# Kernel tuning notes

Measured on AMD Instinct MI355X. Metric: run time of the kernel, lower is better.

## Reference

```python
import jax, jax.numpy as jnp
import numpy as np

N, E, F, H, EA = 50000, 640000, 128, 128, 8


def setup_inputs() -> dict:
    key = jax.random.key(0)
    ks = jax.random.split(key, 16)
    s = 0.05
    return {
        "h": jax.random.normal(ks[0], (N, F), jnp.float32),
        "pos": jax.random.normal(ks[1], (N, 3), jnp.float32),
        "edge_index": jax.random.randint(ks[2], (2, E), 0, N, jnp.int32),
        "edge_attr": jax.random.normal(ks[3], (E, EA), jnp.float32),
        # edge_mlp_1: in = 2F + 1 + EA
        "eW1": jax.random.normal(ks[4], (2 * F + 1 + EA, H), jnp.float32) * s,
        "eb1": jnp.zeros((H,), jnp.float32),
        "eW2": jax.random.normal(ks[5], (H, H), jnp.float32) * s,
        "eb2": jnp.zeros((H,), jnp.float32),
        "aW": jax.random.normal(ks[6], (H, 1), jnp.float32) * s,
        "ab": jnp.zeros((1,), jnp.float32),
        "nW1": jax.random.normal(ks[7], (H + F, H), jnp.float32) * s,
        "nb1": jnp.zeros((H,), jnp.float32),
        "nW2": jax.random.normal(ks[8], (H, F), jnp.float32) * s,
        "nb2": jnp.zeros((F,), jnp.float32),
        # pos_mlp_2: xavier with gain 0.001 -> tiny init, no bias
        "pW2": jax.random.normal(ks[9], (H, 1), jnp.float32) * 0.001,
    }


def reference(h, pos, edge_index, edge_attr,
              eW1, eb1, eW2, eb2, aW, ab,
              nW1, nb1, nW2, nb2, pW2):
    n = h.shape[0]
    row, col = edge_index[0], edge_index[1]
    # radial info
    pos_diff = pos[row] - pos[col]                      # [E,3]
    dist_sq = jnp.sum(pos_diff * pos_diff, axis=-1, keepdims=True)  # [E,1]
    # edge model (Eq.3): gather -> MLP -> sigmoid attention gate
    e_in = jnp.concatenate([h[row], h[col], dist_sq, edge_attr], axis=-1)
    m = jax.nn.silu(e_in @ eW1 + eb1)
    m = jax.nn.silu(m @ eW2 + eb2)
    m = m * jax.nn.sigmoid(m @ aW + ab)                 # [E,H]
    # pos model (note: original overwrites pos_mlp_1 output; faithful to that)
    trans = pos_diff * (m @ pW2)                        # [E,3]
    agg_t = jax.ops.segment_sum(trans, row, num_segments=n)
    cnt = jax.ops.segment_sum(jnp.ones((trans.shape[0], 1), trans.dtype), row,
                              num_segments=n)
    pos_new = pos + agg_t / jnp.maximum(cnt, 1.0)       # unsorted_segment_mean
    # node model: scatter-sum aggregate -> MLP -> residual
    agg = jax.ops.segment_sum(m, row, num_segments=n)   # [N,H]
    o = jax.nn.silu(jnp.concatenate([h, agg], axis=1) @ nW1 + nb1)
    h_new = o @ nW2 + nb2 + h
    return h_new, pos_new, m
```

## Files before the change

### kernel.cpp

```cpp
#include <hip/hip_runtime.h>
#include <hip/hip_bf16.h>

#define NN 50000
#define EE 640000
#define FF 128
#define HH 128

typedef unsigned short ushort_t;
typedef unsigned int   uint_t;
using f32x4  = __attribute__((ext_vector_type(4))) float;
using bf16x8 = __attribute__((ext_vector_type(8))) __bf16;
using u16x8  = __attribute__((ext_vector_type(8))) unsigned short;

__device__ __forceinline__ ushort_t f2bf(float f) {
    union { float f; unsigned int i; } v; v.f = f;
    unsigned int r = v.i + 0x7fffu + ((v.i >> 16) & 1u);
    return (ushort_t)(r >> 16);
}
__device__ __forceinline__ float bf2f(uint_t u) {
    union { uint_t i; float f; } v; v.i = u << 16; return v.f;
}
__device__ __forceinline__ float fsilu(float x) { return x / (1.f + __expf(-x)); }
__device__ __forceinline__ float fsig(float x)  { return 1.f / (1.f + __expf(-x)); }

__device__ __forceinline__ u16x8 cvt8(const float* p) {
    float4 a0 = *reinterpret_cast<const float4*>(p);
    float4 a1 = *reinterpret_cast<const float4*>(p + 4);
    u16x8 v;
    v[0] = f2bf(a0.x); v[1] = f2bf(a0.y); v[2] = f2bf(a0.z); v[3] = f2bf(a0.w);
    v[4] = f2bf(a1.x); v[5] = f2bf(a1.y); v[6] = f2bf(a1.z); v[7] = f2bf(a1.w);
    return v;
}

__global__ void prep_kernel(const float* __restrict__ h, ushort_t* __restrict__ hbf,
                            const int* __restrict__ eidx, int* __restrict__ deg)
{
    const int t = blockIdx.x * 256 + threadIdx.x;
    if (t * 8 < NN * 128) {
        u16x8 v = cvt8(h + (size_t)t * 8);
        *reinterpret_cast<u16x8*>(hbf + (size_t)t * 8) = v;
    }
    if (t < EE) atomicAdd(&deg[eidx[t]], 1);
}

__global__ void scan_kernel(const int* __restrict__ deg, int* __restrict__ row_ptr,
                            int* __restrict__ cursor)
{
    __shared__ int sdata[1024];
    const int t = threadIdx.x;
    const int chunk = (NN + 1023) / 1024;
    const int start = t * chunk;
    const int end   = min(start + chunk, NN);
    int s = 0;
    for (int i = start; i < end; ++i) s += deg[i];
    sdata[t] = s;
    __syncthreads();
    for (int off = 1; off < 1024; off <<= 1) {
        int v = (t >= off) ? sdata[t - off] : 0;
        __syncthreads();
        sdata[t] += v;
        __syncthreads();
    }
    int ox = sdata[t] - s;
    for (int i = start; i < end; ++i) {
        row_ptr[i] = ox; cursor[i] = ox; ox += deg[i];
    }
    if (t == 1023) row_ptr[NN] = sdata[1023];
}

__global__ void scatter_kernel(const int* __restrict__ eidx, int* __restrict__ cursor,
                               int* __restrict__ edge_list, int* __restrict__ row_sorted)
{
    const int e = blockIdx.x * 256 + threadIdx.x;
    if (e < EE) {
        const int r = eidx[e];
        const int p = atomicAdd(&cursor[r], 1);
        edge_list[p] = e;
        row_sorted[p] = r;
    }
}

#define A_STR 288
#define M_STR 136

__device__ __forceinline__ ushort_t* a_ptr(ushort_t* base, int row, int b) {
    const int bs = (b < 512) ? (b ^ ((row & 7) << 4)) : b;
    return base + row * A_STR + (bs >> 1);
}

__global__ __launch_bounds__(256, 2) void egcl_edge_kernel(
    const ushort_t* __restrict__ hbf, const float* __restrict__ pos,
    const int* __restrict__ eidx, const float* __restrict__ eattr,
    const int* __restrict__ edge_list, const int* __restrict__ row_sorted,
    const float* __restrict__ w1, const float* __restrict__ b1,
    const float* __restrict__ w2, const float* __restrict__ b2,
    const float* __restrict__ aW, const float* __restrict__ ab,
    const float* __restrict__ pW2,
    float* __restrict__ m_out, float* __restrict__ agg, float* __restrict__ agg_t)
{
    __shared__ __align__(16) ushort_t A_sh[64 * A_STR];
    __shared__ __align__(16) ushort_t M1_sh[64 * M_STR];
    __shared__ int   ROW_sh[64];
    __shared__ int   EO_sh[64];
    __shared__ float GATE_sh[64];

    ushort_t* M2_sh = A_sh;

    const int tid  = threadIdx.x;
    const int lane = tid & 63;
    const int w    = tid >> 6;
    const int l15  = lane & 15;
    const int lg   = lane >> 4;

    bf16x8 B1[9][2];
    bf16x8 B2[4][2];
    bf16x8 Bg[4];
    float b1c[2], b2c[2];
    const float abv = ab[0];
#pragma unroll
    for (int nt = 0; nt < 2; ++nt) {
        const int colg = 32 * w + 16 * nt + l15;
        b1c[nt] = b1[colg];
        b2c[nt] = b2[colg];
#pragma unroll
        for (int ks = 0; ks < 9; ++ks) {
            u16x8 v;
#pragma unroll
            for (int j = 0; j < 8; ++j) {
                const int k = 32 * ks + 8 * lg + j;
                v[j] = (k < 265) ? f2bf(w1[k * 128 + colg]) : (ushort_t)0;
            }
            B1[ks][nt] = __builtin_bit_cast(bf16x8, v);
        }
#pragma unroll
        for (int ks = 0; ks < 4; ++ks) {
            u16x8 v;
#pragma unroll
            for (int j = 0; j < 8; ++j) {
                const int k = 32 * ks + 8 * lg + j;
                v[j] = f2bf(w2[k * 128 + colg]);
            }
            B2[ks][nt] = __builtin_bit_cast(bf16x8, v);
        }
    }
#pragma unroll
    for (int ks = 0; ks < 4; ++ks) {
        u16x8 v;
#pragma unroll
        for (int j = 0; j < 8; ++j) {
            const int k = 32 * ks + 8 * lg + j;
            v[j] = (l15 == 0) ? f2bf(aW[k]) : (l15 == 1 ? f2bf(pW2[k]) : (ushort_t)0);
        }
        Bg[ks] = __builtin_bit_cast(bf16x8, v);
    }

    const int ei = tid >> 2;
    const int et = tid & 3;

    for (int tile = blockIdx.x; tile < EE / 64; tile += gridDim.x) {
        float pdx = 0.f, pdy = 0.f, pdz = 0.f;
        {
            const int p  = tile * 64 + ei;
            const int eo = edge_list[p];
            const int r  = row_sorted[p];
            const int c  = eidx[EE + eo];
            const ushort_t* hr = hbf + (size_t)r * 128 + et * 32;
            const ushort_t* hc = hbf + (size_t)c * 128 + et * 32;
#pragma unroll
            for (int q = 0; q < 4; ++q) {
                *reinterpret_cast<u16x8*>(a_ptr(A_sh, ei, 64 * et + 16 * q)) =
                    *reinterpret_cast<const u16x8*>(hr + q * 8);
                *reinterpret_cast<u16x8*>(a_ptr(A_sh, ei, 256 + 64 * et + 16 * q)) =
                    *reinterpret_cast<const u16x8*>(hc + q * 8);
            }
            if (et == 0) {
                ROW_sh[ei] = r;
                EO_sh[ei]  = eo;
                pdx = pos[r * 3 + 0] - pos[c * 3 + 0];
                pdy = pos[r * 3 + 1] - pos[c * 3 + 1];
                pdz = pos[r * 3 + 2] - pos[c * 3 + 2];
                const float ds = pdx * pdx + pdy * pdy + pdz * pdz;
                const float4 ea0 = *reinterpret_cast<const float4*>(eattr + (size_t)eo * 8);
                const float4 ea1 = *reinterpret_cast<const float4*>(eattr + (size_t)eo * 8 + 4);
                u16x8 v0;
                v0[0] = f2bf(ds);
                v0[1] = f2bf(ea0.x); v0[2] = f2bf(ea0.y); v0[3] = f2bf(ea0.z);
                v0[4] = f2bf(ea0.w); v0[5] = f2bf(ea1.x); v0[6] = f2bf(ea1.y);
                v0[7] = f2bf(ea1.z);
                *reinterpret_cast<u16x8*>(a_ptr(A_sh, ei, 512)) = v0;
                u16x8 v1 = {0, 0, 0, 0, 0, 0, 0, 0};
                v1[0] = f2bf(ea1.w);
                *reinterpret_cast<u16x8*>(a_ptr(A_sh, ei, 528)) = v1;
                u16x8 z = {0, 0, 0, 0, 0, 0, 0, 0};
                *reinterpret_cast<u16x8*>(a_ptr(A_sh, ei, 544)) = z;
                *reinterpret_cast<u16x8*>(a_ptr(A_sh, ei, 560)) = z;
            }
        }
        __syncthreads();

#pragma unroll
        for (int s = 0; s < 4; ++s) {
            f32x4 a0 = {0.f, 0.f, 0.f, 0.f};
            f32x4 a1 = {0.f, 0.f, 0.f, 0.f};
#pragma unroll
            for (int ks = 0; ks < 9; ++ks) {
                bf16x8 a = *reinterpret_cast<const bf16x8*>(
                    a_ptr(A_sh, 16 * s + l15, 64 * ks + 16 * lg));
                a0 = __builtin_amdgcn_mfma_f32_16x16x32_bf16(a, B1[ks][0], a0, 0, 0, 0);
                a1 = __builtin_amdgcn_mfma_f32_16x16x32_bf16(a, B1[ks][1], a1, 0, 0, 0);
            }
#pragma unroll
            for (int nt = 0; nt < 2; ++nt) {
#pragma unroll
                for (int rr = 0; rr < 4; ++rr) {
                    const float x = (nt == 0 ? a0[rr] : a1[rr]) + b1c[nt];
                    const int edge = 16 * s + 4 * lg + rr;
                    const int colg = 32 * w + 16 * nt + l15;
                    M1_sh[edge * M_STR + colg] = f2bf(fsilu(x));
                }
            }
        }
        __syncthreads();

#pragma unroll
        for (int s = 0; s < 4; ++s) {
            f32x4 a0 = {0.f, 0.f, 0.f, 0.f};
            f32x4 a1 = {0.f, 0.f, 0.f, 0.f};
#pragma unroll
            for (int ks = 0; ks < 4; ++ks) {
                bf16x8 a = *reinterpret_cast<const bf16x8*>(
                    &M1_sh[(16 * s + l15) * M_STR + ks * 32 + lg * 8]);
                a0 = __builtin_amdgcn_mfma_f32_16x16x32_bf16(a, B2[ks][0], a0, 0, 0, 0);
                a1 = __builtin_amdgcn_mfma_f32_16x16x32_bf16(a, B2[ks][1], a1, 0, 0, 0);
            }
#pragma unroll
            for (int nt = 0; nt < 2; ++nt) {
#pragma unroll
                for (int rr = 0; rr < 4; ++rr) {
                    const float x = (nt == 0 ? a0[rr] : a1[rr]) + b2c[nt];
                    const int edge = 16 * s + 4 * lg + rr;
                    const int colg = 32 * w + 16 * nt + l15;
                    M2_sh[edge * M_STR + colg] = f2bf(fsilu(x));
                }
            }
        }
        __syncthreads();

        float gqw[4], txw[4], tyw[4], tzw[4];
        {
            f32x4 ga = {0.f, 0.f, 0.f, 0.f};
#pragma unroll
            for (int ks = 0; ks < 4; ++ks) {
                bf16x8 a = *reinterpret_cast<const bf16x8*>(
                    &M2_sh[(16 * w + l15) * M_STR + ks * 32 + lg * 8]);
                ga = __builtin_amdgcn_mfma_f32_16x16x32_bf16(a, Bg[ks], ga, 0, 0, 0);
            }
#pragma unroll
            for (int rr = 0; rr < 4; ++rr) {
                const float sa = __shfl(ga[rr], lane & 48);
                const float sp = __shfl(ga[rr], (lane & 48) + 1);
                gqw[rr] = fsig(sa + abv);
                const float t = gqw[rr] * sp;
                const float px = __shfl(pdx, 16 * lg + 4 * rr);
                const float py = __shfl(pdy, 16 * lg + 4 * rr);
                const float pz = __shfl(pdz, 16 * lg + 4 * rr);
                txw[rr] = px * t; tyw[rr] = py * t; tzw[rr] = pz * t;
                if (l15 == 0) GATE_sh[16 * w + 4 * lg + rr] = gqw[rr];
            }
            if (l15 == 0) {
                int cur = -1; float t0 = 0.f, t1 = 0.f, t2 = 0.f;
#pragma unroll
                for (int rr = 0; rr < 4; ++rr) {
                    const int rid = ROW_sh[16 * w + 4 * lg + rr];
                    if (rid != cur) {
                        if (cur >= 0) {
                            atomicAdd(&agg_t[cur * 3 + 0], t0);
                            atomicAdd(&agg_t[cur * 3 + 1], t1);
                            atomicAdd(&agg_t[cur * 3 + 2], t2);
                        }
                        cur = rid; t0 = t1 = t2 = 0.f;
                    }
                    t0 += txw[rr]; t1 += tyw[rr]; t2 += tzw[rr];
                }
                atomicAdd(&agg_t[cur * 3 + 0], t0);
                atomicAdd(&agg_t[cur * 3 + 1], t1);
                atomicAdd(&agg_t[cur * 3 + 2], t2);
            }
        }

#pragma unroll
        for (int j = 0; j < 16; ++j) {
            const int row = 16 * w + j;
            const uint_t pv = *reinterpret_cast<const uint_t*>(&M2_sh[row * M_STR + 2 * lane]);
            const float g = __shfl(gqw[j & 3], 16 * (j >> 2));
            float2 st;
            st.x = bf2f(pv & 0xffffu) * g;
            st.y = bf2f(pv >> 16) * g;
            *reinterpret_cast<float2*>(&m_out[(size_t)EO_sh[row] * 128 + 2 * lane]) = st;
        }
        __syncthreads();

        {
            const int col = tid & 127;
            const int j0  = (tid >> 7) * 32;
            int cur = ROW_sh[j0];
            float acc = 0.f;
#pragma unroll 4
            for (int j = j0; j < j0 + 32; ++j) {
                const int rid = ROW_sh[j];
                const float v = bf2f((uint_t)M2_sh[j * M_STR + col]) * GATE_sh[j];
                if (rid != cur) {
                    atomicAdd(&agg[(size_t)cur * 128 + col], acc);
                    acc = 0.f; cur = rid;
                }
                acc += v;
            }
            atomicAdd(&agg[(size_t)cur * 128 + col], acc);
        }
        __syncthreads();
    }
}

__global__ __launch_bounds__(256, 4) void egcl_node_kernel(
    const ushort_t* __restrict__ hbf, const float* __restrict__ h,
    const float* __restrict__ agg, const float* __restrict__ agg_t,
    const int* __restrict__ row_ptr, const float* __restrict__ pos,
    const float* __restrict__ w1, const float* __restrict__ b1,
    const float* __restrict__ w2, const float* __restrict__ b2,
    float* __restrict__ hn_out, float* __restrict__ pos_out)
{
    __shared__ __align__(16) ushort_t A_sh[16 * 264];
    __shared__ __align__(16) ushort_t M1_sh[16 * 136];

    const int tid  = threadIdx.x;
    const int lane = tid & 63;
    const int w    = tid >> 6;
    const int l15  = lane & 15;
    const int lg   = lane >> 4;

    bf16x8 B1[8][2];
    bf16x8 B2[4][2];
    float b1c[2], b2c[2];
#pragma unroll
    for (int nt = 0; nt < 2; ++nt) {
        const int colg = 32 * w + 16 * nt + l15;
        b1c[nt] = b1[colg];
        b2c[nt] = b2[colg];
#pragma unroll
        for (int ks = 0; ks < 8; ++ks) {
            u16x8 v;
#pragma unroll
            for (int j = 0; j < 8; ++j) {
                const int k = 32 * ks + 8 * lg + j;
                v[j] = f2bf(w1[k * 128 + colg]);
            }
            B1[ks][nt] = __builtin_bit_cast(bf16x8, v);
        }
#pragma unroll
        for (int ks = 0; ks < 4; ++ks) {
            u16x8 v;
#pragma unroll
            for (int j = 0; j < 8; ++j) {
                const int k = 32 * ks + 8 * lg + j;
                v[j] = f2bf(w2[k * 128 + colg]);
            }
            B2[ks][nt] = __builtin_bit_cast(bf16x8, v);
        }
    }

    const int ni = tid >> 4;
    const int nt16 = tid & 15;

    for (int tile = blockIdx.x; tile < NN / 16; tile += gridDim.x) {
        __syncthreads();
        const int base = tile * 16;
        {
            const size_t n = (size_t)base + ni;
            *reinterpret_cast<u16x8*>(&A_sh[ni * 264 + nt16 * 8]) =
                *reinterpret_cast<const u16x8*>(hbf + n * 128 + nt16 * 8);
            u16x8 av = cvt8(agg + n * 128 + nt16 * 8);
            *reinterpret_cast<u16x8*>(&A_sh[ni * 264 + 128 + nt16 * 8]) = av;
        }
        if (tid < 48) {
            const int nl = tid / 3, d = tid % 3;
            const size_t n = (size_t)base + nl;
            const float c = (float)(row_ptr[n + 1] - row_ptr[n]);
            pos_out[n * 3 + d] = pos[n * 3 + d] + agg_t[n * 3 + d] / fmaxf(c, 1.f);
        }
        __syncthreads();

        f32x4 acc10 = {0.f, 0.f, 0.f, 0.f};
        f32x4 acc11 = {0.f, 0.f, 0.f, 0.f};
#pragma unroll
        for (int ks = 0; ks < 8; ++ks) {
            bf16x8 a = *reinterpret_cast<const bf16x8*>(&A_sh[l15 * 264 + ks * 32 + lg * 8]);
            acc10 = __builtin_amdgcn_mfma_f32_16x16x32_bf16(a, B1[ks][0], acc10, 0, 0, 0);
            acc11 = __builtin_amdgcn_mfma_f32_16x16x32_bf16(a, B1[ks][1], acc11, 0, 0, 0);
        }
#pragma unroll
        for (int nt = 0; nt < 2; ++nt) {
#pragma unroll
            for (int r = 0; r < 4; ++r) {
                const float x = (nt == 0 ? acc10[r] : acc11[r]) + b1c[nt];
                const int nl = 4 * lg + r;
                const int colg = 32 * w + 16 * nt + l15;
                M1_sh[nl * 136 + colg] = f2bf(fsilu(x));
            }
        }
        __syncthreads();

        f32x4 acc20 = {0.f, 0.f, 0.f, 0.f};
        f32x4 acc21 = {0.f, 0.f, 0.f, 0.f};
#pragma unroll
        for (int ks = 0; ks < 4; ++ks) {
            bf16x8 a = *reinterpret_cast<const bf16x8*>(&M1_sh[l15 * 136 + ks * 32 + lg * 8]);
            acc20 = __builtin_amdgcn_mfma_f32_16x16x32_bf16(a, B2[ks][0], acc20, 0, 0, 0);
            acc21 = __builtin_amdgcn_mfma_f32_16x16x32_bf16(a, B2[ks][1], acc21, 0, 0, 0);
        }
#pragma unroll
        for (int nt = 0; nt < 2; ++nt) {
#pragma unroll
            for (int r = 0; r < 4; ++r) {
                const int nl = 4 * lg + r;
                const int colg = 32 * w + 16 * nt + l15;
                const size_t n = (size_t)base + nl;
                const float hres = h[n * 128 + colg];
                const float y = (nt == 0 ? acc20[r] : acc21[r]) + b2c[nt] + hres;
                hn_out[n * 128 + colg] = y;
            }
        }
    }
}

extern "C" void kernel_launch(void* const* d_in, const int* in_sizes, int n_in,
                              void* d_out, int out_size, void* d_ws, size_t ws_size,
                              hipStream_t stream)
{
    const float* h     = (const float*)d_in[0];
    const float* pos   = (const float*)d_in[1];
    const int*   eidx  = (const int*)d_in[2];
    const float* eattr = (const float*)d_in[3];
    const float* eW1   = (const float*)d_in[4];
    const float* eb1   = (const float*)d_in[5];
    const float* eW2   = (const float*)d_in[6];
    const float* eb2   = (const float*)d_in[7];
    const float* aW    = (const float*)d_in[8];
    const float* ab    = (const float*)d_in[9];
    const float* nW1   = (const float*)d_in[10];
    const float* nb1   = (const float*)d_in[11];
    const float* nW2   = (const float*)d_in[12];
    const float* nb2   = (const float*)d_in[13];
    const float* pW2   = (const float*)d_in[14];

    float* out    = (float*)d_out;
    float* hn_out = out;
    float* po_out = out + (size_t)NN * 128;
    float* m_out  = po_out + (size_t)NN * 3;

    char* wsb = (char*)d_ws;
    float* agg        = (float*)(wsb + 0);
    float* agg_t      = (float*)(wsb + 25600000);
    int*   deg        = (int*)  (wsb + 26200000);
    int*   row_ptr    = (int*)  (wsb + 26400000);
    int*   cursor     = (int*)  (wsb + 26600256);
    int*   edge_list  = (int*)  (wsb + 26800256);
    int*   row_sorted = (int*)  (wsb + 29360256);
    ushort_t* hbf     = (ushort_t*)(wsb + 31920256);

    hipMemsetAsync(wsb, 0, 26400000, stream);

    prep_kernel<<<3200, 256, 0, stream>>>(h, hbf, eidx, deg);
    scan_kernel<<<1, 1024, 0, stream>>>(deg, row_ptr, cursor);
    scatter_kernel<<<(EE + 255) / 256, 256, 0, stream>>>(eidx, cursor, edge_list, row_sorted);

    egcl_edge_kernel<<<512, 256, 0, stream>>>(hbf, pos, eidx, eattr,
                                              edge_list, row_sorted,
                                              eW1, eb1, eW2, eb2, aW, ab, pW2,
                                              m_out, agg, agg_t);
    egcl_node_kernel<<<1024, 256, 0, stream>>>(hbf, h, agg, agg_t, row_ptr, pos,
                                               nW1, nb1, nW2, nb2,
                                               hn_out, po_out);
}
```

Before: 539.6 us.

## Use 512-thread edge blocks with one 16-column MFMA tile per wave

The edge kernel now runs 8 waves per block instead of 4. Each wave owns a single 16-column output slice, which halves the per-thread weight registers and MFMA accumulators, and gather work is spread across 8 threads per edge. The gate and position-scale values now go through shared memory via a new SP_sh buffer, the m_out store loop reads edge_list directly, and the scatter-sum segments shrink to 16 rows. This adds one extra barrier and the m_out write no longer has a barrier before the aggregation, in exchange for more waves to hide gather and atomic latency.

Result: slower. 619.1 us (+14.7%).

```diff
diff --git a/kernel.cpp b/kernel.cpp
--- a/kernel.cpp
+++ b/kernel.cpp
@@ -88,7 +88,7 @@
     return base + row * A_STR + (bs >> 1);
 }
 
-__global__ __launch_bounds__(256, 2) void egcl_edge_kernel(
+__global__ __launch_bounds__(512) void egcl_edge_kernel(
     const ushort_t* __restrict__ hbf, const float* __restrict__ pos,
     const int* __restrict__ eidx, const float* __restrict__ eattr,
     const int* __restrict__ edge_list, const int* __restrict__ row_sorted,
@@ -101,8 +101,8 @@
     __shared__ __align__(16) ushort_t A_sh[64 * A_STR];
     __shared__ __align__(16) ushort_t M1_sh[64 * M_STR];
     __shared__ int   ROW_sh[64];
-    __shared__ int   EO_sh[64];
     __shared__ float GATE_sh[64];
+    __shared__ float SP_sh[64];
 
     ushort_t* M2_sh = A_sh;
 
@@ -112,36 +112,32 @@
     const int l15  = lane & 15;
     const int lg   = lane >> 4;
 
-    bf16x8 B1[9][2];
-    bf16x8 B2[4][2];
+    bf16x8 B1[9];
+    bf16x8 B2[4];
     bf16x8 Bg[4];
-    float b1c[2], b2c[2];
+    const int colg = 16 * w + l15;
+    const float b1c = b1[colg];
+    const float b2c = b2[colg];
     const float abv = ab[0];
 #pragma unroll
-    for (int nt = 0; nt < 2; ++nt) {
-        const int colg = 32 * w + 16 * nt + l15;
-        b1c[nt] = b1[colg];
-        b2c[nt] = b2[colg];
-#pragma unroll
-        for (int ks = 0; ks < 9; ++ks) {
-            u16x8 v;
-#pragma unroll
-            for (int j = 0; j < 8; ++j) {
-                const int k = 32 * ks + 8 * lg + j;
-                v[j] = (k < 265) ? f2bf(w1[k * 128 + colg]) : (ushort_t)0;
-            }
-            B1[ks][nt] = __builtin_bit_cast(bf16x8, v);
-        }
-#pragma unroll
-        for (int ks = 0; ks < 4; ++ks) {
-            u16x8 v;
-#pragma unroll
-            for (int j = 0; j < 8; ++j) {
-                const int k = 32 * ks + 8 * lg + j;
-                v[j] = f2bf(w2[k * 128 + colg]);
-            }
-            B2[ks][nt] = __builtin_bit_cast(bf16x8, v);
-        }
+    for (int ks = 0; ks < 9; ++ks) {
+        u16x8 v;
+#pragma unroll
+        for (int j = 0; j < 8; ++j) {
+            const int k = 32 * ks + 8 * lg + j;
+            v[j] = (k < 265) ? f2bf(w1[k * 128 + colg]) : (ushort_t)0;
+        }
+        B1[ks] = __builtin_bit_cast(bf16x8, v);
+    }
+#pragma unroll
+    for (int ks = 0; ks < 4; ++ks) {
+        u16x8 v;
+#pragma unroll
+        for (int j = 0; j < 8; ++j) {
+            const int k = 32 * ks + 8 * lg + j;
+            v[j] = f2bf(w2[k * 128 + colg]);
+        }
+        B2[ks] = __builtin_bit_cast(bf16x8, v);
     }
 #pragma unroll
     for (int ks = 0; ks < 4; ++ks) {
@@ -154,8 +150,8 @@
         Bg[ks] = __builtin_bit_cast(bf16x8, v);
     }
 
-    const int ei = tid >> 2;
-    const int et = tid & 3;
+    const int ei = tid >> 3;
+    const int et = tid & 7;
 
     for (int tile = blockIdx.x; tile < EE / 64; tile += gridDim.x) {
         float pdx = 0.f, pdy = 0.f, pdz = 0.f;
@@ -164,18 +160,17 @@
             const int eo = edge_list[p];
             const int r  = row_sorted[p];
             const int c  = eidx[EE + eo];
-            const ushort_t* hr = hbf + (size_t)r * 128 + et * 32;
-            const ushort_t* hc = hbf + (size_t)c * 128 + et * 32;
-#pragma unroll
-            for (int q = 0; q < 4; ++q) {
-                *reinterpret_cast<u16x8*>(a_ptr(A_sh, ei, 64 * et + 16 * q)) =
+            const ushort_t* hr = hbf + (size_t)r * 128 + et * 16;
+            const ushort_t* hc = hbf + (size_t)c * 128 + et * 16;
+#pragma unroll
+            for (int q = 0; q < 2; ++q) {
+                *reinterpret_cast<u16x8*>(a_ptr(A_sh, ei, 32 * et + 16 * q)) =
                     *reinterpret_cast<const u16x8*>(hr + q * 8);
-                *reinterpret_cast<u16x8*>(a_ptr(A_sh, ei, 256 + 64 * et + 16 * q)) =
+                *reinterpret_cast<u16x8*>(a_ptr(A_sh, ei, 256 + 32 * et + 16 * q)) =
                     *reinterpret_cast<const u16x8*>(hc + q * 8);
             }
             if (et == 0) {
                 ROW_sh[ei] = r;
-                EO_sh[ei]  = eo;
                 pdx = pos[r * 3 + 0] - pos[c * 3 + 0];
                 pdy = pos[r * 3 + 1] - pos[c * 3 + 1];
                 pdz = pos[r * 3 + 2] - pos[c * 3 + 2];
@@ -201,23 +196,17 @@
 #pragma unroll
         for (int s = 0; s < 4; ++s) {
             f32x4 a0 = {0.f, 0.f, 0.f, 0.f};
-            f32x4 a1 = {0.f, 0.f, 0.f, 0.f};
 #pragma unroll
             for (int ks = 0; ks < 9; ++ks) {
                 bf16x8 a = *reinterpret_cast<const bf16x8*>(
                     a_ptr(A_sh, 16 * s + l15, 64 * ks + 16 * lg));
-                a0 = __builtin_amdgcn_mfma_f32_16x16x32_bf16(a, B1[ks][0], a0, 0, 0, 0);
-                a1 = __builtin_amdgcn_mfma_f32_16x16x32_bf16(a, B1[ks][1], a1, 0, 0, 0);
-            }
-#pragma unroll
-            for (int nt = 0; nt < 2; ++nt) {
-#pragma unroll
-                for (int rr = 0; rr < 4; ++rr) {
-                    const float x = (nt == 0 ? a0[rr] : a1[rr]) + b1c[nt];
-                    const int edge = 16 * s + 4 * lg + rr;
-                    const int colg = 32 * w + 16 * nt + l15;
-                    M1_sh[edge * M_STR + colg] = f2bf(fsilu(x));
-                }
+                a0 = __builtin_amdgcn_mfma_f32_16x16x32_bf16(a, B1[ks], a0, 0, 0, 0);
+            }
+#pragma unroll
+            for (int rr = 0; rr < 4; ++rr) {
+                const float x = a0[rr] + b1c;
+                const int edge = 16 * s + 4 * lg + rr;
+                M1_sh[edge * M_STR + colg] = f2bf(fsilu(x));
             }
         }
         __syncthreads();
@@ -225,29 +214,22 @@
 #pragma unroll
         for (int s = 0; s < 4; ++s) {
             f32x4 a0 = {0.f, 0.f, 0.f, 0.f};
-            f32x4 a1 = {0.f, 0.f, 0.f, 0.f};
 #pragma unroll
             for (int ks = 0; ks < 4; ++ks) {
                 bf16x8 a = *reinterpret_cast<const bf16x8*>(
                     &M1_sh[(16 * s + l15) * M_STR + ks * 32 + lg * 8]);
-                a0 = __builtin_amdgcn_mfma_f32_16x16x32_bf16(a, B2[ks][0], a0, 0, 0, 0);
-                a1 = __builtin_amdgcn_mfma_f32_16x16x32_bf16(a, B2[ks][1], a1, 0, 0, 0);
-            }
-#pragma unroll
-            for (int nt = 0; nt < 2; ++nt) {
-#pragma unroll
-                for (int rr = 0; rr < 4; ++rr) {
-                    const float x = (nt == 0 ? a0[rr] : a1[rr]) + b2c[nt];
-                    const int edge = 16 * s + 4 * lg + rr;
-                    const int colg = 32 * w + 16 * nt + l15;
-                    M2_sh[edge * M_STR + colg] = f2bf(fsilu(x));
-                }
-            }
-        }
-        __syncthreads();
-
-        float gqw[4], txw[4], tyw[4], tzw[4];
-        {
+                a0 = __builtin_amdgcn_mfma_f32_16x16x32_bf16(a, B2[ks], a0, 0, 0, 0);
+            }
+#pragma unroll
+            for (int rr = 0; rr < 4; ++rr) {
+                const float x = a0[rr] + b2c;
+                const int edge = 16 * s + 4 * lg + rr;
+                M2_sh[edge * M_STR + colg] = f2bf(fsilu(x));
+            }
+        }
+        __syncthreads();
+
+        if (w < 4) {
             f32x4 ga = {0.f, 0.f, 0.f, 0.f};
 #pragma unroll
             for (int ks = 0; ks < 4; ++ks) {
@@ -259,19 +241,42 @@
             for (int rr = 0; rr < 4; ++rr) {
                 const float sa = __shfl(ga[rr], lane & 48);
                 const float sp = __shfl(ga[rr], (lane & 48) + 1);
-                gqw[rr] = fsig(sa + abv);
-                const float t = gqw[rr] * sp;
-                const float px = __shfl(pdx, 16 * lg + 4 * rr);
-                const float py = __shfl(pdy, 16 * lg + 4 * rr);
-                const float pz = __shfl(pdz, 16 * lg + 4 * rr);
-                txw[rr] = px * t; tyw[rr] = py * t; tzw[rr] = pz * t;
-                if (l15 == 0) GATE_sh[16 * w + 4 * lg + rr] = gqw[rr];
-            }
-            if (l15 == 0) {
+                if (l15 == 0) {
+                    const int edge = 16 * w + 4 * lg + rr;
+                    GATE_sh[edge] = fsig(sa + abv);
+                    SP_sh[edge]   = sp;
+                }
+            }
+        }
+        __syncthreads();
+
+#pragma unroll
+        for (int j = 0; j < 8; ++j) {
+            const int row = 8 * w + j;
+            const int eo  = edge_list[tile * 64 + row];
+            const uint_t pv = *reinterpret_cast<const uint_t*>(&M2_sh[row * M_STR + 2 * lane]);
+            const float g = GATE_sh[row];
+            float2 st;
+            st.x = bf2f(pv & 0xffffu) * g;
+            st.y = bf2f(pv >> 16) * g;
+            *reinterpret_cast<float2*>(&m_out[(size_t)eo * 128 + 2 * lane]) = st;
+        }
+
+        {
+            float px[8], py[8], pz[8];
+#pragma unroll
+            for (int j = 0; j < 8; ++j) {
+                px[j] = __shfl(pdx, 8 * j);
+                py[j] = __shfl(pdy, 8 * j);
+                pz[j] = __shfl(pdz, 8 * j);
+            }
+            if (lane == 0) {
                 int cur = -1; float t0 = 0.f, t1 = 0.f, t2 = 0.f;
 #pragma unroll
-                for (int rr = 0; rr < 4; ++rr) {
-                    const int rid = ROW_sh[16 * w + 4 * lg + rr];
+                for (int j = 0; j < 8; ++j) {
+                    const int e = 8 * w + j;
+                    const int rid = ROW_sh[e];
+                    const float t = GATE_sh[e] * SP_sh[e];
                     if (rid != cur) {
                         if (cur >= 0) {
                             atomicAdd(&agg_t[cur * 3 + 0], t0);
@@ -280,7 +285,7 @@
                         }
                         cur = rid; t0 = t1 = t2 = 0.f;
                     }
-                    t0 += txw[rr]; t1 += tyw[rr]; t2 += tzw[rr];
+                    t0 += px[j] * t; t1 += py[j] * t; t2 += pz[j] * t;
                 }
                 atomicAdd(&agg_t[cur * 3 + 0], t0);
                 atomicAdd(&agg_t[cur * 3 + 1], t1);
@@ -288,25 +293,13 @@
             }
         }
 
-#pragma unroll
-        for (int j = 0; j < 16; ++j) {
-            const int row = 16 * w + j;
-            const uint_t pv = *reinterpret_cast<const uint_t*>(&M2_sh[row * M_STR + 2 * lane]);
-            const float g = __shfl(gqw[j & 3], 16 * (j >> 2));
-            float2 st;
-            st.x = bf2f(pv & 0xffffu) * g;
-            st.y = bf2f(pv >> 16) * g;
-            *reinterpret_cast<float2*>(&m_out[(size_t)EO_sh[row] * 128 + 2 * lane]) = st;
-        }
-        __syncthreads();
-
         {
             const int col = tid & 127;
-            const int j0  = (tid >> 7) * 32;
+            const int j0  = (tid >> 7) * 16;
             int cur = ROW_sh[j0];
             float acc = 0.f;
 #pragma unroll 4
-            for (int j = j0; j < j0 + 32; ++j) {
+            for (int j = j0; j < j0 + 16; ++j) {
                 const int rid = ROW_sh[j];
                 const float v = bf2f((uint_t)M2_sh[j * M_STR + col]) * GATE_sh[j];
                 if (rid != cur) {
@@ -473,7 +466,7 @@
     scan_kernel<<<1, 1024, 0, stream>>>(deg, row_ptr, cursor);
     scatter_kernel<<<(EE + 255) / 256, 256, 0, stream>>>(eidx, cursor, edge_list, row_sorted);
 
-    egcl_edge_kernel<<<512, 256, 0, stream>>>(hbf, pos, eidx, eattr,
+    egcl_edge_kernel<<<512, 512, 0, stream>>>(hbf, pos, eidx, eattr,
                                               edge_list, row_sorted,
                                               eW1, eb1, eW2, eb2, aW, ab, pW2,
                                               m_out, agg, agg_t);
```
